# Performance work log

Hardware: AMD Instinct MI355X
Metric: run time of the kernel (lower is better)

Reference implementation:

```python
import jax, jax.numpy as jnp
import numpy as np

K = 5            # neighborhood kernel size
PAD = 2
CENTER = (K * K) // 2   # index 12: the pixel itself
TEMP = 0.1       # InfoNCE temperature
EPS = 1e-8
NUM_CLASSES = 2


def _patches_f(x):
    """x: [B,H,W,C] float -> [B,H,W,K*K,C] zero-padded 5x5 neighborhoods."""
    B, H, W, C = x.shape
    xp = jnp.pad(x, ((0, 0), (PAD, PAD), (PAD, PAD), (0, 0)))
    return jnp.stack([xp[:, i:i + H, j:j + W, :]
                      for i in range(K) for j in range(K)], axis=3)


def _patches_i(x):
    """x: [B,H,W] int -> [B,H,W,K*K] zero-padded 5x5 neighborhoods."""
    B, H, W = x.shape
    xp = jnp.pad(x, ((0, 0), (PAD, PAD), (PAD, PAD)))
    return jnp.stack([xp[:, i:i + H, j:j + W]
                      for i in range(K) for j in range(K)], axis=3)


def setup_inputs() -> dict:
    key = jax.random.key(0)
    k1, k2, k3, k4 = jax.random.split(key, 4)
    B, C, H, W = 2, 256, 96, 96
    return {
        "er_input": jax.random.normal(k1, (B, C, H, W), dtype=jnp.float32),
        "seg_logit": jax.random.normal(k2, (B, NUM_CLASSES, H, W), dtype=jnp.float32),
        "seg_label": jax.random.randint(k3, (B, H, W), 0, NUM_CLASSES, dtype=jnp.int32),
        "gt_boundary_seg": jax.random.randint(k4, (B, H, W), 0, 2, dtype=jnp.int32),
    }


def reference(er_input, seg_logit, seg_label, gt_boundary_seg):
    # er_input: [B,C,H,W]; seg_logit: [B,nc,H,W]; labels: [B,H,W]
    feat = er_input.transpose(0, 2, 3, 1)          # [B,H,W,C]
    pred = jnp.argmax(seg_logit, axis=1)           # [B,H,W]
    gt_b = jnp.where(gt_boundary_seg == 255, 0, gt_boundary_seg)
    edge = gt_b.astype(bool)                       # boundary mask [B,H,W]

    neigh_feat = _patches_f(feat)                  # [B,H,W,25,C]
    neigh_label = _patches_i(seg_label)            # [B,H,W,25]
    neigh_pred = _patches_i(pred)                  # [B,H,W,25]

    def correct(c):
        # one_hot(label)*one_hot(pred) at class c, per neighbor
        return ((neigh_label == c) & (neigh_pred == c)).astype(feat.dtype)

    a_norm_neigh = jnp.linalg.norm(neigh_feat, axis=-1)   # [B,H,W,25]

    total = jnp.asarray(0.0, dtype=feat.dtype)
    shown = list(range(NUM_CLASSES))               # shown_class (both assumed present)
    n_cls = len(shown)
    for i in range(n_cls):
        c = shown[i]
        c_pre = shown[(i - 1) % n_cls]
        c_post = shown[(i + 1) % n_cls]

        now_mask = (seg_label == c)                # [B,H,W]
        neigh_is_c = (neigh_label == c).astype(feat.dtype)
        # same-class neighbor count, center excluded (kernel has 0 at center)
        count = neigh_is_c.sum(-1) - neigh_is_c[..., CENTER]
        pix_mask = ((count >= 1) & edge & now_mask).astype(feat.dtype)  # [B,H,W]

        w_now = correct(c)                         # [B,H,W,25]
        w_neg = correct(c_pre) + correct(c_post)   # pre_class + post_class weights

        # anchor = center feature * correct indicator (taken before zeroing center)
        anchor = neigh_feat[..., CENTER, :] * w_now[..., CENTER, None]  # [B,H,W,C]
        # positive = mean over 25 neighbors of (feat * correct), center zeroed
        positive = (jnp.einsum('bhwkc,bhwk->bhwc', neigh_feat, w_now) - anchor) / (K * K)

        a_norm = jnp.linalg.norm(anchor, axis=-1)  # [B,H,W]
        p_norm = jnp.linalg.norm(positive, axis=-1)
        pos_cos = (anchor * positive).sum(-1) / (a_norm * p_norm + EPS)   # [B,H,W]

        # negatives: per-offset features weighted by (pre+post) correctness
        dots = jnp.einsum('bhwc,bhwkc->bhwk', anchor, neigh_feat)         # [B,H,W,25]
        neg_cos = (dots * w_neg) / (a_norm[..., None] * a_norm_neigh * w_neg + EPS)

        logits = jnp.concatenate([pos_cos[..., None], neg_cos], axis=-1) / TEMP
        loss_pix = -jax.nn.log_softmax(logits, axis=-1)[..., 0]          # [B,H,W]

        total = total + (loss_pix * pix_mask).sum() / jnp.maximum(pix_mask.sum(), 1.0)
    return total
```

## Files before the change

kernel.cpp:

```cpp
#include <hip/hip_runtime.h>
#include <math.h>

#define Hc 96
#define Wc 96
#define Bc 2
#define Cc 256
#define HWc (Hc * Wc)
#define NKc 25
#define NPIX (Bc * HWc)
#define NSLOT 32

#define OFF_ACC 0
#define OFF_CNT 256
#define OFF_MIS 264
#define OFF_HC 272
#define OFF_DONE 276
#define HDR_FLOATS 80
#define OFF_NRM2 320
#define OFF_META (OFF_NRM2 + 2 * NPIX * 4)
#define OFF_WL (OFF_META + NPIX)
#define OFF_FT (OFF_WL + NPIX * 16)

__device__ __forceinline__ float wave_reduce_sum(float v) {
#pragma unroll
  for (int off = 32; off > 0; off >>= 1) v += __shfl_xor(v, off);
  return v;
}

#define NOFF(k) (((k) / 5 - 2) * Wc + ((k) % 5 - 2))

__device__ __forceinline__ unsigned f2bf_pack(float lo, float hi) {
  unsigned a = __float_as_uint(lo), b = __float_as_uint(hi);
  a = (a + 0x7FFFu + ((a >> 16) & 1u)) >> 16;
  b = (b + 0x7FFFu + ((b >> 16) & 1u)) >> 16;
  return a | (b << 16);
}
__device__ __forceinline__ float bf2f(unsigned short u) {
  return __uint_as_float(((unsigned)u) << 16);
}

__global__ __launch_bounds__(256) void transpose_kernel(
    const float* __restrict__ in, const float* __restrict__ seg_logit,
    const int* __restrict__ seg_label, unsigned* __restrict__ outb,
    float* __restrict__ nrm2h, unsigned char* __restrict__ meta,
    float* __restrict__ hdr) {
  __shared__ float tile[64][33];
  __shared__ float part[8][32];
  const int bx = blockIdx.x;
  const int b = blockIdx.y;
  const int half = blockIdx.z;
  const int tx = threadIdx.x;
  const int ty = threadIdx.y;
  const float* src = in + (size_t)b * Cc * HWc;
  const int p0 = bx * 32;

  if (bx == 0 && b == 0 && half == 0) {
    const int t = ty * 32 + tx;
    if (t < HDR_FLOATS) hdr[t] = 0.f;
  }

  float psum = 0.f;
  for (int s = 0; s < 2; ++s) {
    const int c0 = half * 128 + s * 64;
#pragma unroll
    for (int i = 0; i < 8; i++)
      tile[ty + i * 8][tx] = src[(size_t)(c0 + ty + i * 8) * HWc + p0 + tx];
    __syncthreads();
#pragma unroll
    for (int i = 0; i < 4; i++) {
      const int px = ty + i * 8;
      const unsigned pk = f2bf_pack(tile[2 * tx][px], tile[2 * tx + 1][px]);
      outb[(size_t)(b * HWc + p0 + px) * (Cc / 2) + (c0 / 2) + tx] = pk;
    }
#pragma unroll
    for (int j = 0; j < 8; j++) {
      const float v = tile[ty * 8 + j][tx];
      psum += v * v;
    }
    __syncthreads();
  }
  part[ty][tx] = psum;
  __syncthreads();
  if (ty == 0) {
    float t = 0.f;
#pragma unroll
    for (int j = 0; j < 8; j++) t += part[j][tx];
    const int hw = p0 + tx;
    const int gi = b * HWc + hw;
    nrm2h[half * NPIX + gi] = t;
    if (half == 0) {
      const float l0 = seg_logit[(size_t)(b * 2 + 0) * HWc + hw];
      const float l1 = seg_logit[(size_t)(b * 2 + 1) * HWc + hw];
      const int pr = (l1 > l0) ? 1 : 0;
      meta[gi] = (unsigned char)((seg_label[gi] & 1) | (pr << 1));
    }
  }
}

__global__ __launch_bounds__(256) void classify_kernel(
    const unsigned char* __restrict__ meta, const int* __restrict__ gtb,
    const float* __restrict__ nrm2h, float* __restrict__ cnt,
    float* __restrict__ mis, unsigned int* __restrict__ heavyCount,
    uint4* __restrict__ worklist) {
  __shared__ unsigned int s_cnt[4];
  if (threadIdx.x < 4) s_cnt[threadIdx.x] = 0;
  __syncthreads();
  const int tid = blockIdx.x * 256 + threadIdx.x;
  bool heavy = false;
  int c = 0;
  unsigned mNow = 0, mNeg = 0;
  float a_norm = 0.f;
  {
    const int hw = tid % HWc;
    const int h = hw / Wc, w = hw % Wc;
    int g = gtb[tid];
    if (g == 255) g = 0;
    if (g) {
      const int m0 = meta[tid];
      c = m0 & 1;
      const int pc = (m0 >> 1) & 1;
      const int oc = 1 - c;
      int count = 0;
#pragma unroll
      for (int k = 0; k < NKc; k++) {
        const int di = k / 5 - 2, dj = k % 5 - 2;
        const int hh = h + di, ww = w + dj;
        const bool inb = (hh >= 0) && (hh < Hc) && (ww >= 0) && (ww < Wc);
        const int mv = inb ? (int)meta[tid + di * Wc + dj] : 0;
        const int lb = mv & 1, pr = (mv >> 1) & 1;
        count += (lb == c);
        if (inb) {
          if (lb == c && pr == c) mNow |= 1u << k;
          if (lb == oc && pr == oc) mNeg |= 1u << k;
        }
      }
      count -= 1;
      if (count >= 1) {
        atomicAdd(&s_cnt[c], 1u);
        if (pc == c) {
          heavy = true;
          a_norm = sqrtf(nrm2h[tid] + nrm2h[NPIX + tid]);
        } else {
          atomicAdd(&s_cnt[2 + c], 1u);
        }
      }
    }
  }
  const unsigned long long m = __ballot(heavy);
  const int lane = threadIdx.x & 63;
  if (m) {
    unsigned int base = 0;
    if (lane == 0) base = atomicAdd(heavyCount, (unsigned)__popcll(m));
    base = __shfl(base, 0);
    if (heavy) {
      const unsigned idx = base + (unsigned)__popcll(m & ((1ull << lane) - 1ull));
      worklist[idx] = make_uint4((unsigned)tid | ((unsigned)c << 16), mNow, mNeg,
                                 __float_as_uint(a_norm));
    }
  }
  __syncthreads();
  if (threadIdx.x < 2) {
    if (s_cnt[threadIdx.x]) atomicAdd(&cnt[threadIdx.x], (float)s_cnt[threadIdx.x]);
    if (s_cnt[2 + threadIdx.x]) atomicAdd(&mis[threadIdx.x], (float)s_cnt[2 + threadIdx.x]);
  }
}

__global__ __launch_bounds__(256) void heavy_kernel(
    const ushort4* __restrict__ ftb, const float* __restrict__ nrm2h,
    const unsigned int* __restrict__ heavyCount,
    const uint4* __restrict__ worklist, float* __restrict__ accum,
    unsigned int* __restrict__ doneCnt, const float* __restrict__ cnt,
    const float* __restrict__ mis, float* __restrict__ out) {
  __shared__ float s_loss[2];
  __shared__ unsigned s_last;
  if (threadIdx.x < 2) s_loss[threadIdx.x] = 0.f;
  __syncthreads();
  const int lane = threadIdx.x & 63;
  const int wv = threadIdx.x >> 6;
  const unsigned nH = *heavyCount;
  const unsigned nw = gridDim.x * 4;
  float lacc0 = 0.f, lacc1 = 0.f;
  for (unsigned i = blockIdx.x * 4 + wv; i < nH; i += nw) {
    const uint4 e = worklist[i];
    const int wid = e.x & 0xffff;
    const int c = (e.x >> 16) & 1;
    const unsigned mNow = e.y, mNeg = e.z;
    const unsigned mAny = mNow | mNeg;
    const float a_norm = __uint_as_float(e.w);

    float nkv = 0.f;
    if (lane < NKc && ((mNeg >> lane) & 1u)) {
      const int nb = wid + (lane / 5 - 2) * Wc + (lane % 5 - 2);
      nkv = sqrtf(nrm2h[nb] + nrm2h[NPIX + nb]);
    }

    const ushort4 a4 = ftb[(size_t)wid * 64 + lane];
    const float ax = bf2f(a4.x), ay = bf2f(a4.y), az = bf2f(a4.z), aw = bf2f(a4.w);

    ushort4 f4[NKc];
#pragma unroll
    for (int k = 0; k < NKc; k++) {
      f4[k] = make_ushort4(0, 0, 0, 0);
      if ((mAny >> k) & 1u)
        f4[k] = ftb[(size_t)(wid + NOFF(k)) * 64 + lane];
    }
    float4 pos = make_float4(0.f, 0.f, 0.f, 0.f);
    float dpart[NKc];
#pragma unroll
    for (int k = 0; k < NKc; k++) {
      const float fx = bf2f(f4[k].x), fy = bf2f(f4[k].y);
      const float fz = bf2f(f4[k].z), fw = bf2f(f4[k].w);
      const float wN = (float)((mNow >> k) & 1u);
      pos.x = fmaf(fx, wN, pos.x);
      pos.y = fmaf(fy, wN, pos.y);
      pos.z = fmaf(fz, wN, pos.z);
      pos.w = fmaf(fw, wN, pos.w);
      dpart[k] = ax * fx + ay * fy + az * fz + aw * fw;
    }

    float4 pv;
    pv.x = (pos.x - ax) * (1.0f / 25.0f);
    pv.y = (pos.y - ay) * (1.0f / 25.0f);
    pv.z = (pos.z - az) * (1.0f / 25.0f);
    pv.w = (pos.w - aw) * (1.0f / 25.0f);
    const float p2 = wave_reduce_sum(pv.x * pv.x + pv.y * pv.y + pv.z * pv.z + pv.w * pv.w);
    const float ad = wave_reduce_sum(ax * pv.x + ay * pv.y + az * pv.z + aw * pv.w);
    const float x0 = (ad / (a_norm * sqrtf(p2) + 1e-8f)) * 10.0f;
    float mx = fmaxf(x0, 0.f);
#pragma unroll
    for (int k = 0; k < NKc; k++) {
      if ((mNeg >> k) & 1u) {
        const float d = wave_reduce_sum(dpart[k]);
        const float nk = __shfl(nkv, k);
        dpart[k] = ((d * 2.0f) / (a_norm * nk * 2.0f + 1e-8f)) * 10.0f;
        mx = fmaxf(mx, dpart[k]);
      }
    }
    float s = expf(x0 - mx) + (float)(NKc - __popc(mNeg)) * expf(-mx);
#pragma unroll
    for (int k = 0; k < NKc; k++)
      if ((mNeg >> k) & 1u) s += expf(dpart[k] - mx);
    const float loss = mx + logf(s) - x0;
    if (lane == 0) {
      if (c == 0) lacc0 += loss; else lacc1 += loss;
    }
  }
  if (lane == 0) {
    if (lacc0 != 0.f) atomicAdd(&s_loss[0], lacc0);
    if (lacc1 != 0.f) atomicAdd(&s_loss[1], lacc1);
  }
  __syncthreads();
  if (threadIdx.x < 2) {
    const float v = s_loss[threadIdx.x];
    if (v != 0.f) atomicAdd(&accum[(blockIdx.x & (NSLOT - 1)) * 2 + threadIdx.x], v);
  }
  __syncthreads();
  if (threadIdx.x == 0)
    s_last = (atomicAdd(doneCnt, 1u) == (unsigned)(gridDim.x - 1)) ? 1u : 0u;
  __syncthreads();
  if (s_last && threadIdx.x < NSLOT * 2) {
    const float v = atomicAdd(&accum[threadIdx.x], 0.0f);
    float v0 = (threadIdx.x & 1) ? 0.f : v;
    float v1 = (threadIdx.x & 1) ? v : 0.f;
    v0 = wave_reduce_sum(v0);
    v1 = wave_reduce_sum(v1);
    if (threadIdx.x == 0) {
      const float LOG26 = logf(26.0f);
      out[0] = (v0 + LOG26 * mis[0]) / fmaxf(cnt[0], 1.0f) +
               (v1 + LOG26 * mis[1]) / fmaxf(cnt[1], 1.0f);
    }
  }
}

extern "C" void kernel_launch(void* const* d_in, const int* in_sizes, int n_in,
                              void* d_out, int out_size, void* d_ws, size_t ws_size,
                              hipStream_t stream) {
  const float* er = (const float*)d_in[0];
  const float* seg_logit = (const float*)d_in[1];
  const int* seg_label = (const int*)d_in[2];
  const int* gtb = (const int*)d_in[3];
  float* out = (float*)d_out;

  char* ws = (char*)d_ws;
  float* hdr = (float*)ws;
  float* accum = (float*)(ws + OFF_ACC);
  float* cnt = (float*)(ws + OFF_CNT);
  float* mis = (float*)(ws + OFF_MIS);
  unsigned int* heavyCount = (unsigned int*)(ws + OFF_HC);
  unsigned int* doneCnt = (unsigned int*)(ws + OFF_DONE);
  float* nrm2h = (float*)(ws + OFF_NRM2);
  unsigned char* meta = (unsigned char*)(ws + OFF_META);
  uint4* worklist = (uint4*)(ws + OFF_WL);
  unsigned* featTb = (unsigned*)(ws + OFF_FT);

  dim3 tb(32, 8, 1);
  dim3 tg(HWc / 32, Bc, 2);
  transpose_kernel<<<tg, tb, 0, stream>>>(er, seg_logit, seg_label, featTb,
                                          nrm2h, meta, hdr);

  classify_kernel<<<NPIX / 256, 256, 0, stream>>>(meta, gtb, nrm2h, cnt, mis,
                                                  heavyCount, worklist);

  heavy_kernel<<<1152, 256, 0, stream>>>((const ushort4*)featTb, nrm2h,
                                         heavyCount, worklist, accum, doneCnt,
                                         cnt, mis, out);
}
```

Before: 49.60 us.

## Fuse classify and heavy kernels with per-block shared-memory worklist

Merges the pixel classification kernel and the heavy loss kernel into one launch. One wavefront classifies 32 pixels per block and writes the selected heavy pixels into a shared-memory worklist. The four waves of the block then process that list. This removes a kernel launch, the global worklist writes and reads, and the global heavy-count atomic. Per-class counters are now updated with wave ballots instead of shared atomics. In exchange, load balance depends on how many heavy pixels land in each 32-pixel block, and three waves sit idle during classification.

```diff
diff --git a/kernel.cpp b/kernel.cpp
--- a/kernel.cpp
+++ b/kernel.cpp
@@ -9,17 +9,17 @@
 #define NKc 25
 #define NPIX (Bc * HWc)
 #define NSLOT 32
+#define PXB 32
+#define NFB (NPIX / PXB)
 
 #define OFF_ACC 0
 #define OFF_CNT 256
 #define OFF_MIS 264
-#define OFF_HC 272
 #define OFF_DONE 276
 #define HDR_FLOATS 80
 #define OFF_NRM2 320
 #define OFF_META (OFF_NRM2 + 2 * NPIX * 4)
-#define OFF_WL (OFF_META + NPIX)
-#define OFF_FT (OFF_WL + NPIX * 16)
+#define OFF_FT (OFF_META + NPIX)
 
 __device__ __forceinline__ float wave_reduce_sum(float v) {
 #pragma unroll
@@ -97,91 +97,86 @@
   }
 }
 
-__global__ __launch_bounds__(256) void classify_kernel(
+__global__ __launch_bounds__(256) void fused_kernel(
+    const ushort4* __restrict__ ftb, const float* __restrict__ nrm2h,
     const unsigned char* __restrict__ meta, const int* __restrict__ gtb,
-    const float* __restrict__ nrm2h, float* __restrict__ cnt,
-    float* __restrict__ mis, unsigned int* __restrict__ heavyCount,
-    uint4* __restrict__ worklist) {
-  __shared__ unsigned int s_cnt[4];
-  if (threadIdx.x < 4) s_cnt[threadIdx.x] = 0;
-  __syncthreads();
-  const int tid = blockIdx.x * 256 + threadIdx.x;
-  bool heavy = false;
-  int c = 0;
-  unsigned mNow = 0, mNeg = 0;
-  float a_norm = 0.f;
-  {
-    const int hw = tid % HWc;
-    const int h = hw / Wc, w = hw % Wc;
-    int g = gtb[tid];
-    if (g == 255) g = 0;
-    if (g) {
-      const int m0 = meta[tid];
-      c = m0 & 1;
-      const int pc = (m0 >> 1) & 1;
-      const int oc = 1 - c;
-      int count = 0;
-#pragma unroll
-      for (int k = 0; k < NKc; k++) {
-        const int di = k / 5 - 2, dj = k % 5 - 2;
-        const int hh = h + di, ww = w + dj;
-        const bool inb = (hh >= 0) && (hh < Hc) && (ww >= 0) && (ww < Wc);
-        const int mv = inb ? (int)meta[tid + di * Wc + dj] : 0;
-        const int lb = mv & 1, pr = (mv >> 1) & 1;
-        count += (lb == c);
-        if (inb) {
-          if (lb == c && pr == c) mNow |= 1u << k;
-          if (lb == oc && pr == oc) mNeg |= 1u << k;
+    float* __restrict__ accum, float* __restrict__ cnt,
+    float* __restrict__ mis, unsigned int* __restrict__ doneCnt,
+    float* __restrict__ out) {
+  __shared__ uint4 s_wl[PXB];
+  __shared__ int s_nH;
+  __shared__ float s_loss[2];
+  __shared__ unsigned s_last;
+  const int lane = threadIdx.x & 63;
+  const int wv = threadIdx.x >> 6;
+  if (threadIdx.x < 2) s_loss[threadIdx.x] = 0.f;
+
+  if (wv == 0) {
+    bool heavy = false, contrib = false, mispred = false;
+    int c = 0;
+    unsigned mNow = 0, mNeg = 0;
+    float a_norm = 0.f;
+    const int tid = blockIdx.x * PXB + lane;
+    if (lane < PXB) {
+      const int hw = tid % HWc;
+      const int h = hw / Wc, w = hw % Wc;
+      int g = gtb[tid];
+      if (g == 255) g = 0;
+      if (g) {
+        const int m0 = meta[tid];
+        c = m0 & 1;
+        const int pc = (m0 >> 1) & 1;
+        const int oc = 1 - c;
+        int count = 0;
+#pragma unroll
+        for (int k = 0; k < NKc; k++) {
+          const int di = k / 5 - 2, dj = k % 5 - 2;
+          const int hh = h + di, ww = w + dj;
+          const bool inb = (hh >= 0) && (hh < Hc) && (ww >= 0) && (ww < Wc);
+          const int mv = inb ? (int)meta[tid + di * Wc + dj] : 0;
+          const int lb = mv & 1, pr = (mv >> 1) & 1;
+          count += (lb == c);
+          if (inb) {
+            if (lb == c && pr == c) mNow |= 1u << k;
+            if (lb == oc && pr == oc) mNeg |= 1u << k;
+          }
+        }
+        count -= 1;
+        if (count >= 1) {
+          contrib = true;
+          if (pc == c) {
+            heavy = true;
+            a_norm = sqrtf(nrm2h[tid] + nrm2h[NPIX + tid]);
+          } else {
+            mispred = true;
+          }
         }
       }
-      count -= 1;
-      if (count >= 1) {
-        atomicAdd(&s_cnt[c], 1u);
-        if (pc == c) {
-          heavy = true;
-          a_norm = sqrtf(nrm2h[tid] + nrm2h[NPIX + tid]);
-        } else {
-          atomicAdd(&s_cnt[2 + c], 1u);
-        }
-      }
-    }
-  }
-  const unsigned long long m = __ballot(heavy);
-  const int lane = threadIdx.x & 63;
-  if (m) {
-    unsigned int base = 0;
-    if (lane == 0) base = atomicAdd(heavyCount, (unsigned)__popcll(m));
-    base = __shfl(base, 0);
+    }
+    const unsigned long long bc0 = __ballot(contrib && c == 0);
+    const unsigned long long bc1 = __ballot(contrib && c == 1);
+    const unsigned long long bm0 = __ballot(mispred && c == 0);
+    const unsigned long long bm1 = __ballot(mispred && c == 1);
+    const unsigned long long bh = __ballot(heavy);
+    if (lane == 0) {
+      if (bc0) atomicAdd(&cnt[0], (float)__popcll(bc0));
+      if (bc1) atomicAdd(&cnt[1], (float)__popcll(bc1));
+      if (bm0) atomicAdd(&mis[0], (float)__popcll(bm0));
+      if (bm1) atomicAdd(&mis[1], (float)__popcll(bm1));
+      s_nH = __popcll(bh);
+    }
     if (heavy) {
-      const unsigned idx = base + (unsigned)__popcll(m & ((1ull << lane) - 1ull));
-      worklist[idx] = make_uint4((unsigned)tid | ((unsigned)c << 16), mNow, mNeg,
-                                 __float_as_uint(a_norm));
-    }
-  }
-  __syncthreads();
-  if (threadIdx.x < 2) {
-    if (s_cnt[threadIdx.x]) atomicAdd(&cnt[threadIdx.x], (float)s_cnt[threadIdx.x]);
-    if (s_cnt[2 + threadIdx.x]) atomicAdd(&mis[threadIdx.x], (float)s_cnt[2 + threadIdx.x]);
-  }
-}
-
-__global__ __launch_bounds__(256) void heavy_kernel(
-    const ushort4* __restrict__ ftb, const float* __restrict__ nrm2h,
-    const unsigned int* __restrict__ heavyCount,
-    const uint4* __restrict__ worklist, float* __restrict__ accum,
-    unsigned int* __restrict__ doneCnt, const float* __restrict__ cnt,
-    const float* __restrict__ mis, float* __restrict__ out) {
-  __shared__ float s_loss[2];
-  __shared__ unsigned s_last;
-  if (threadIdx.x < 2) s_loss[threadIdx.x] = 0.f;
-  __syncthreads();
-  const int lane = threadIdx.x & 63;
-  const int wv = threadIdx.x >> 6;
-  const unsigned nH = *heavyCount;
-  const unsigned nw = gridDim.x * 4;
+      const int idx = __popcll(bh & ((1ull << lane) - 1ull));
+      s_wl[idx] = make_uint4((unsigned)tid | ((unsigned)c << 16), mNow, mNeg,
+                             __float_as_uint(a_norm));
+    }
+  }
+  __syncthreads();
+
+  const int nH = s_nH;
   float lacc0 = 0.f, lacc1 = 0.f;
-  for (unsigned i = blockIdx.x * 4 + wv; i < nH; i += nw) {
-    const uint4 e = worklist[i];
+  for (int i = wv; i < nH; i += 4) {
+    const uint4 e = s_wl[i];
     const int wid = e.x & 0xffff;
     const int c = (e.x >> 16) & 1;
     const unsigned mNow = e.y, mNeg = e.z;
@@ -286,11 +281,9 @@
   float* accum = (float*)(ws + OFF_ACC);
   float* cnt = (float*)(ws + OFF_CNT);
   float* mis = (float*)(ws + OFF_MIS);
-  unsigned int* heavyCount = (unsigned int*)(ws + OFF_HC);
   unsigned int* doneCnt = (unsigned int*)(ws + OFF_DONE);
   float* nrm2h = (float*)(ws + OFF_NRM2);
   unsigned char* meta = (unsigned char*)(ws + OFF_META);
-  uint4* worklist = (uint4*)(ws + OFF_WL);
   unsigned* featTb = (unsigned*)(ws + OFF_FT);
 
   dim3 tb(32, 8, 1);
@@ -298,10 +291,6 @@
   transpose_kernel<<<tg, tb, 0, stream>>>(er, seg_logit, seg_label, featTb,
                                           nrm2h, meta, hdr);
 
-  classify_kernel<<<NPIX / 256, 256, 0, stream>>>(meta, gtb, nrm2h, cnt, mis,
-                                                  heavyCount, worklist);
-
-  heavy_kernel<<<1152, 256, 0, stream>>>((const ushort4*)featTb, nrm2h,
-                                         heavyCount, worklist, accum, doneCnt,
-                                         cnt, mis, out);
-}
+  fused_kernel<<<NFB, 256, 0, stream>>>((const ushort4*)featTb, nrm2h, meta,
+                                        gtb, accum, cnt, mis, doneCnt, out);
+}
```

New measurement: 75.56 us. +52.3%, slower.
